# Optimization experiments

Measured on AMD Instinct MI355X. Metric: run time of the kernel, lower is better.

Reference implementation:

```python
import jax, jax.numpy as jnp
import numpy as np

NUM_TERMS = 8192  # weight shape: [num_terms-1, 2*num_terms-2]


def setup_inputs() -> dict:
    key = jax.random.key(0)
    weight = jax.random.normal(key, (NUM_TERMS - 1, 2 * NUM_TERMS - 2), dtype=jnp.float32)
    return {"weight": weight}


def reference(weight) -> jnp.ndarray:
    rows, cols = weight.shape
    num_terms = rows + 1
    # Original: keep entries where num_terms + i > j, else set to 0 (after abs).
    i = jnp.arange(rows)[:, None]          # [rows, 1]
    j = jnp.arange(cols)[None, :]          # [1, cols]
    keep = (num_terms + i) > j             # [rows, cols] boolean mask
    W = jnp.where(keep, jnp.abs(weight), jnp.zeros((), dtype=weight.dtype))
    # Softmax over dim=1 INCLUDING the zeroed entries (zeros contribute e^0=1),
    # exactly matching torch.softmax(W, dim=1) on the masked matrix.
    return jax.nn.softmax(W, axis=1)
```

## Files before the change

### kernel.cpp

```cpp
#include <hip/hip_runtime.h>

#define ROWS 8191
#define COLS 16382
#define NT   8192

__global__ __launch_bounds__(1024) void masked_softmax_kernel(
    const float* __restrict__ w, float* __restrict__ out) {
    __shared__ float redsum[16];

    const int row = blockIdx.x;
    const int tid = threadIdx.x;
    const size_t base = (size_t)row * COLS;
    const float* wr   = w + base;
    float*       outr = out + base;
    const int limit   = NT + row;

    float e[16];
    float lsum = 0.0f;

    #pragma unroll
    for (int it = 0; it < 8; ++it) {
        const int j = (it * 1024 + tid) * 2;
        float2 v = make_float2(0.0f, 0.0f);
        const bool in0 = (j     < COLS);
        if (in0) v = *reinterpret_cast<const float2*>(wr + j);
        const float a0 = (j     < limit) ? fabsf(v.x) : 0.0f;
        const float a1 = (j + 1 < limit) ? fabsf(v.y) : 0.0f;
        float e0 = __expf(a0);
        float e1 = __expf(a1);
        if (!in0) { e0 = 0.0f; e1 = 0.0f; }
        e[2 * it]     = e0;
        e[2 * it + 1] = e1;
        lsum += e0 + e1;
    }

    #pragma unroll
    for (int off = 32; off; off >>= 1)
        lsum += __shfl_xor(lsum, off, 64);
    if ((tid & 63) == 0)
        redsum[tid >> 6] = lsum;
    __syncthreads();
    float s = 0.0f;
    #pragma unroll
    for (int k = 0; k < 16; ++k)
        s += redsum[k];
    const float inv = 1.0f / s;

    #pragma unroll
    for (int it = 0; it < 8; ++it) {
        const int j = (it * 1024 + tid) * 2;
        if (j < COLS) {
            float2 o;
            o.x = e[2 * it]     * inv;
            o.y = e[2 * it + 1] * inv;
            *reinterpret_cast<float2*>(outr + j) = o;
        }
    }
}

extern "C" void kernel_launch(void* const* d_in, const int* in_sizes, int n_in,
                              void* d_out, int out_size, void* d_ws, size_t ws_size,
                              hipStream_t stream) {
    const float* w = (const float*)d_in[0];
    float* out = (float*)d_out;
    masked_softmax_kernel<<<ROWS, 1024, 0, stream>>>(w, out);
}
```

Measured before the change: 210.5 us.

## Process two rows per block with 16-byte nontemporal loads and stores

```diff
diff --git a/kernel.cpp b/kernel.cpp
--- a/kernel.cpp
+++ b/kernel.cpp
@@ -4,56 +4,93 @@
 #define COLS 16382
 #define NT   8192
 
-__global__ __launch_bounds__(1024) void masked_softmax_kernel(
+typedef float f32x4 __attribute__((ext_vector_type(4)));
+
+__global__ __launch_bounds__(1024, 8) void masked_softmax_kernel(
     const float* __restrict__ w, float* __restrict__ out) {
-    __shared__ float redsum[16];
+    __shared__ float redA[16], redB[16];
 
-    const int row = blockIdx.x;
+    const int b   = blockIdx.x;
     const int tid = threadIdx.x;
-    const size_t base = (size_t)row * COLS;
-    const float* wr   = w + base;
-    float*       outr = out + base;
-    const int limit   = NT + row;
+    const bool hasB = (b != 4095);
+    const int rowA = 2 * b;
+    const size_t base = (size_t)rowA * COLS;
+    const float* wp = w + base;
+    float*       op = out + base;
+    const int limitA = NT + rowA;
+    const int limitB = limitA + 1;
+    const int nvalid = hasB ? 2 * COLS : COLS;
 
-    float e[16];
-    float lsum = 0.0f;
+    float e[32];
+    float sumA = 0.0f, sumB = 0.0f;
 
     #pragma unroll
     for (int it = 0; it < 8; ++it) {
-        const int j = (it * 1024 + tid) * 2;
-        float2 v = make_float2(0.0f, 0.0f);
-        const bool in0 = (j     < COLS);
-        if (in0) v = *reinterpret_cast<const float2*>(wr + j);
-        const float a0 = (j     < limit) ? fabsf(v.x) : 0.0f;
-        const float a1 = (j + 1 < limit) ? fabsf(v.y) : 0.0f;
-        float e0 = __expf(a0);
-        float e1 = __expf(a1);
-        if (!in0) { e0 = 0.0f; e1 = 0.0f; }
-        e[2 * it]     = e0;
-        e[2 * it + 1] = e1;
-        lsum += e0 + e1;
+        const int p = (it * 1024 + tid) * 4;
+        if (p + 3 < nvalid) {
+            const f32x4 v = __builtin_nontemporal_load(
+                reinterpret_cast<const f32x4*>(wp + p));
+            #pragma unroll
+            for (int m = 0; m < 4; ++m) {
+                const int  pe  = p + m;
+                const bool isB = (pe >= COLS);
+                const int  col = isB ? (pe - COLS) : pe;
+                const int  lim = isB ? limitB : limitA;
+                const float a  = (col < lim) ? fabsf(v[m]) : 0.0f;
+                const float ex = __expf(a);
+                e[it * 4 + m] = ex;
+                sumA += isB ? 0.0f : ex;
+                sumB += isB ? ex : 0.0f;
+            }
+        } else {
+            #pragma unroll
+            for (int m = 0; m < 4; ++m) {
+                const int pe = p + m;
+                float ex = 0.0f;
+                if (pe < nvalid) {
+                    const float x  = wp[pe];
+                    const bool isB = (pe >= COLS);
+                    const int  col = isB ? (pe - COLS) : pe;
+                    const int  lim = isB ? limitB : limitA;
+                    const float a  = (col < lim) ? fabsf(x) : 0.0f;
+                    ex = __expf(a);
+                    if (isB) sumB += ex; else sumA += ex;
+                }
+                e[it * 4 + m] = ex;
+            }
+        }
     }
 
     #pragma unroll
-    for (int off = 32; off; off >>= 1)
-        lsum += __shfl_xor(lsum, off, 64);
-    if ((tid & 63) == 0)
-        redsum[tid >> 6] = lsum;
+    for (int off = 32; off; off >>= 1) {
+        sumA += __shfl_xor(sumA, off, 64);
+        sumB += __shfl_xor(sumB, off, 64);
+    }
+    if ((tid & 63) == 0) { redA[tid >> 6] = sumA; redB[tid >> 6] = sumB; }
     __syncthreads();
-    float s = 0.0f;
+    float sA = 0.0f, sB = 0.0f;
     #pragma unroll
-    for (int k = 0; k < 16; ++k)
-        s += redsum[k];
-    const float inv = 1.0f / s;
+    for (int k = 0; k < 16; ++k) { sA += redA[k]; sB += redB[k]; }
+    const float invA = 1.0f / sA;
+    const float invB = 1.0f / sB;
 
     #pragma unroll
     for (int it = 0; it < 8; ++it) {
-        const int j = (it * 1024 + tid) * 2;
-        if (j < COLS) {
-            float2 o;
-            o.x = e[2 * it]     * inv;
-            o.y = e[2 * it + 1] * inv;
-            *reinterpret_cast<float2*>(outr + j) = o;
+        const int p = (it * 1024 + tid) * 4;
+        if (p + 3 < nvalid) {
+            f32x4 o;
+            o[0] = e[it * 4 + 0] * ((p + 0 >= COLS) ? invB : invA);
+            o[1] = e[it * 4 + 1] * ((p + 1 >= COLS) ? invB : invA);
+            o[2] = e[it * 4 + 2] * ((p + 2 >= COLS) ? invB : invA);
+            o[3] = e[it * 4 + 3] * ((p + 3 >= COLS) ? invB : invA);
+            __builtin_nontemporal_store(o, reinterpret_cast<f32x4*>(op + p));
+        } else {
+            #pragma unroll
+            for (int m = 0; m < 4; ++m) {
+                const int pe = p + m;
+                if (pe < nvalid)
+                    op[pe] = e[it * 4 + m] * ((pe >= COLS) ? invB : invA);
+            }
         }
     }
 }
@@ -63,5 +100,5 @@
                               hipStream_t stream) {
     const float* w = (const float*)d_in[0];
     float* out = (float*)d_out;
-    masked_softmax_kernel<<<ROWS, 1024, 0, stream>>>(w, out);
+    masked_softmax_kernel<<<4096, 1024, 0, stream>>>(w, out);
 }
```

Result: faster. 201.6 us (-4.2%).
